# Performance work log

Measured on AMD Instinct MI355X. Metric: run time of the kernel, lower is better.

## Reference

```python
import jax, jax.numpy as jnp
import numpy as np

NUM_ENTITIES = 100000
NUM_RELATIONS = 500
D = 256            # embedding_dim
T = 4              # num_hash_tables
H = 32             # hash_dim
B = 64             # batch of queries
K = 10
CAND = max(K * 10, int(NUM_ENTITIES * 0.1))  # = 10000


def setup_inputs() -> dict:
    key = jax.random.key(0)
    k0, k1, k2, k3, k4 = jax.random.split(key, 5)
    return {
        "head": jax.random.randint(k0, (B,), 0, NUM_ENTITIES),
        "relation": jax.random.randint(k1, (B,), 0, NUM_RELATIONS),
        "entity_emb": jax.random.normal(k2, (NUM_ENTITIES, D), jnp.float32) * 0.02,
        "relation_emb": jax.random.normal(k3, (NUM_RELATIONS, D), jnp.float32) * 0.02,
        "hash_proj": jax.random.normal(k4, (T, D, H), jnp.float32),
        "k": K,
    }


def reference(head, relation, entity_emb, relation_emb, hash_proj, k):
    # DistMult approximate query path of KnowledgeGraph.query (use_approximate=True).
    h = entity_emb[head]            # [B, D]
    r = relation_emb[relation]      # [B, D]
    target = h * r                  # DistMult target embedding [B, D]

    # LSH hash codes (0/1 floats): projected > 0
    thash = (jnp.einsum('bd,tdh->bth', target, hash_proj) > 0).astype(jnp.float32)      # [B,T,H]
    ahash = (jnp.einsum('nd,tdh->nth', entity_emb, hash_proj) > 0).astype(jnp.float32)  # [N,T,H]

    # Hamming distance over (T,H) bits without materializing [B,N,T,H]:
    # mismatches = sum(a) + sum(b) - 2 * <a,b>  for 0/1 codes
    dot = jnp.einsum('bth,nth->bn', thash, ahash)                                        # [B,N]
    hash_dist = thash.sum((1, 2))[:, None] + ahash.sum((1, 2))[None, :] - 2.0 * dot      # [B,N]

    # top num_candidates with SMALLEST hamming distance
    _, cand_idx = jax.lax.top_k(-hash_dist, CAND)                                        # [B,CAND]

    # DistMult score: (h*r*t).sum(-1) == target . t ; compute dense then gather candidates
    scores_all = jnp.einsum('bd,nd->bn', target, entity_emb)                             # [B,N]
    cand_scores = jnp.take_along_axis(scores_all, cand_idx, axis=1)                      # [B,CAND]

    top_scores, top_local = jax.lax.top_k(cand_scores, k)                                # [B,k]
    top_indices = jnp.take_along_axis(cand_idx, top_local, axis=1)                       # [B,k]
    return top_indices, top_scores
```

## Files before the change

### kernel.cpp

```cpp
#include <hip/hip_runtime.h>
#include <hip/hip_bf16.h>
#include <float.h>

constexpr int NENT  = 100000;
constexpr int DDIM  = 256;
constexpr int BQ    = 64;
constexpr int CANDN = 10000;
constexpr int KTOP  = 10;
constexpr int NSLICE = 16;
constexpr int SLICE  = 6272;
constexpr int HPAD   = 132;

typedef short v8s __attribute__((ext_vector_type(8)));
typedef float v4f __attribute__((ext_vector_type(4)));

__device__ inline void split3(float x, unsigned short& h0, unsigned short& h1,
                              unsigned short& h2) {
    unsigned t0 = __float_as_uint(x) & 0xffff0000u;
    float r1 = x - __uint_as_float(t0);
    unsigned t1 = __float_as_uint(r1) & 0xffff0000u;
    float r2 = r1 - __uint_as_float(t1);
    h0 = (unsigned short)(t0 >> 16);
    h1 = (unsigned short)(t1 >> 16);
    h2 = (unsigned short)(__float_as_uint(r2) >> 16);
}

__device__ inline void split8(const float* ap, v8s& o0, v8s& o1, v8s& o2) {
    union { v8s v; unsigned short u[8]; } r0, r1, r2;
    float4 f0 = *(const float4*)ap;
    float4 f1 = *(const float4*)(ap + 4);
    float av[8] = {f0.x, f0.y, f0.z, f0.w, f1.x, f1.y, f1.z, f1.w};
    #pragma unroll
    for (int j = 0; j < 8; j++)
        split3(av[j], r0.u[j], r1.u[j], r2.u[j]);
    o0 = r0.v; o1 = r1.v; o2 = r2.v;
}

__global__ __launch_bounds__(128) void k_targets(
    const int* __restrict__ head, const int* __restrict__ rel,
    const float* __restrict__ E, const float* __restrict__ Rm,
    const float* __restrict__ proj,
    float* __restrict__ tgtT, unsigned* __restrict__ thash)
{
    __shared__ float tg[DDIM];
    int b = blockIdx.x;
    int tid = threadIdx.x;
    int h = head[b], r = rel[b];
    for (int d = tid; d < DDIM; d += 128) {
        float v = E[h*DDIM + d] * Rm[r*DDIM + d];
        tg[d] = v;
        tgtT[d*BQ + b] = v;
    }
    __syncthreads();
    int t = tid >> 5, hh = tid & 31;
    float acc = 0.f;
    #pragma unroll 8
    for (int d = 0; d < DDIM; d++)
        acc += tg[d] * proj[(t*DDIM + d)*32 + hh];
    unsigned long long m = __ballot(acc > 0.0f);
    int lane = tid & 63, w = tid >> 6;
    if (lane == 0) {
        thash[b*4 + w*2 + 0] = (unsigned)(m & 0xffffffffull);
        thash[b*4 + w*2 + 1] = (unsigned)(m >> 32);
    }
}

__global__ __launch_bounds__(256) void k_prepw(
    const float* __restrict__ proj, const float* __restrict__ tgtT,
    unsigned short* __restrict__ Whi, unsigned short* __restrict__ Wmid,
    unsigned short* __restrict__ Wlo)
{
    int c = blockIdx.x;
    int d = threadIdx.x;
    float x = (c < 128) ? proj[((c >> 5)*DDIM + d)*32 + (c & 31)]
                        : tgtT[d*BQ + (c - 128)];
    unsigned short h0, h1, h2;
    split3(x, h0, h1, h2);
    Whi [c*DDIM + d] = h0;
    Wmid[c*DDIM + d] = h1;
    Wlo [c*DDIM + d] = h2;
}

constexpr int TILE_E = 128;
constexpr int LSTR = 40;
constexpr int ASTR = 36;

__global__ __launch_bounds__(256, 2) void k_gemm(
    const float* __restrict__ E,
    const unsigned short* __restrict__ Whi, const unsigned short* __restrict__ Wmid,
    const unsigned short* __restrict__ Wlo,
    unsigned* __restrict__ ahash, float* __restrict__ scores)
{
    __shared__ __align__(16) float Af[TILE_E*ASTR];
    __shared__ __align__(16) unsigned short Bhi[192*LSTR];
    __shared__ __align__(16) unsigned short Bmid[192*LSTR];
    __shared__ __align__(16) unsigned short Blo[192*LSTR];
    unsigned short* bitsHalf = (unsigned short*)Af;

    int tid = threadIdx.x;
    int l = tid & 63, w = tid >> 6;
    int wm = w >> 1, wn = w & 1;
    int m = l & 15, quad = l >> 4;
    int n0 = blockIdx.x * TILE_E;

    v4f acc[4][6];
    #pragma unroll
    for (int a = 0; a < 4; a++)
        #pragma unroll
        for (int c = 0; c < 6; c++)
            acc[a][c] = (v4f)0.0f;

    for (int ch = 0; ch < DDIM/32; ch++) {
        int d0 = ch * 32;
        __syncthreads();
        #pragma unroll
        for (int it = 0; it < 4; it++) {
            int idx = tid + it*256;
            int row = idx >> 3;
            int kq  = (idx & 7) * 4;
            int n = n0 + row; if (n >= NENT) n = NENT - 1;
            *(float4*)&Af[row*ASTR + kq] = *(const float4*)(E + (size_t)n*DDIM + d0 + kq);
        }
        #pragma unroll
        for (int it = 0; it < 3; it++) {
            int idx = tid + it*256;
            int col = idx >> 2;
            int k8  = (idx & 3) * 8;
            *(uint4*)&Bhi [col*LSTR + k8] = *(const uint4*)(Whi  + col*DDIM + d0 + k8);
            *(uint4*)&Bmid[col*LSTR + k8] = *(const uint4*)(Wmid + col*DDIM + d0 + k8);
            *(uint4*)&Blo [col*LSTR + k8] = *(const uint4*)(Wlo  + col*DDIM + d0 + k8);
        }
        __syncthreads();
        v8s a0[4], a1[4], a2[4];
        #pragma unroll
        for (int a = 0; a < 4; a++)
            split8(&Af[(wm*64 + a*16 + m)*ASTR + quad*8], a0[a], a1[a], a2[a]);
        #pragma unroll
        for (int c = 0; c < 6; c++) {
            int co = (wn*96 + c*16 + m)*LSTR + quad*8;
            v8s b0 = *(const v8s*)&Bhi [co];
            v8s b1 = *(const v8s*)&Bmid[co];
            v8s b2 = *(const v8s*)&Blo [co];
            #pragma unroll
            for (int a = 0; a < 4; a++) {
                acc[a][c] = __builtin_amdgcn_mfma_f32_16x16x32_bf16(a2[a], b0, acc[a][c], 0, 0, 0);
                acc[a][c] = __builtin_amdgcn_mfma_f32_16x16x32_bf16(a0[a], b2, acc[a][c], 0, 0, 0);
                acc[a][c] = __builtin_amdgcn_mfma_f32_16x16x32_bf16(a1[a], b1, acc[a][c], 0, 0, 0);
                acc[a][c] = __builtin_amdgcn_mfma_f32_16x16x32_bf16(a1[a], b0, acc[a][c], 0, 0, 0);
                acc[a][c] = __builtin_amdgcn_mfma_f32_16x16x32_bf16(a0[a], b1, acc[a][c], 0, 0, 0);
                acc[a][c] = __builtin_amdgcn_mfma_f32_16x16x32_bf16(a0[a], b0, acc[a][c], 0, 0, 0);
            }
        }
    }

    __syncthreads();
    #pragma unroll
    for (int c = 0; c < 6; c++) {
        int ct = wn*6 + c;
        if (ct < 8) {
            #pragma unroll
            for (int a = 0; a < 4; a++) {
                #pragma unroll
                for (int r = 0; r < 4; r++) {
                    unsigned long long mb = __ballot(acc[a][c][r] > 0.0f);
                    if (m == 0) {
                        int rowl = wm*64 + a*16 + quad*4 + r;
                        bitsHalf[rowl*8 + ct] = (unsigned short)(mb >> (quad*16));
                    }
                }
            }
        } else {
            int b = ct*16 - 128 + m;
            #pragma unroll
            for (int a = 0; a < 4; a++) {
                int nb = n0 + wm*64 + a*16 + quad*4;
                if (nb < NENT)
                    *(float4*)(scores + (size_t)b*NENT + nb) = *(float4*)&acc[a][c];
            }
        }
    }
    __syncthreads();
    if (tid < TILE_E) {
        int n = n0 + tid;
        if (n < NENT)
            *(uint4*)(ahash + (size_t)n*4) = *(const uint4*)&bitsHalf[tid*8];
    }
}

__global__ __launch_bounds__(256) void k_dist(
    const unsigned* __restrict__ ahash, const unsigned* __restrict__ thash,
    unsigned char* __restrict__ dist8, unsigned short* __restrict__ histG)
{
    __shared__ unsigned hist[HPAD];
    int s = blockIdx.x, b = blockIdx.y, tid = threadIdx.x;
    for (int i = tid; i < HPAD; i += 256) hist[i] = 0u;
    uint4 tw = *(const uint4*)(thash + b*4);
    __syncthreads();
    int n0 = s*SLICE;
    int n1 = n0 + SLICE; if (n1 > NENT) n1 = NENT;
    unsigned char* drow = dist8 + (size_t)b*NENT;
    for (int n = n0 + tid*4; n < n1; n += 1024) {
        int dv[4];
        #pragma unroll
        for (int i = 0; i < 4; i++) {
            uint4 a = *(const uint4*)(ahash + (size_t)(n+i)*4);
            dv[i] = __popc(a.x^tw.x) + __popc(a.y^tw.y) +
                    __popc(a.z^tw.z) + __popc(a.w^tw.w);
            atomicAdd(&hist[dv[i]], 1u);
        }
        uchar4 o = make_uchar4((unsigned char)dv[0], (unsigned char)dv[1],
                               (unsigned char)dv[2], (unsigned char)dv[3]);
        *(uchar4*)(drow + n) = o;
    }
    __syncthreads();
    unsigned short* hrow = histG + ((size_t)b*NSLICE + s)*HPAD;
    for (int i = tid; i < 129; i += 256) hrow[i] = (unsigned short)hist[i];
}

__global__ __launch_bounds__(64) void k_cut(
    const unsigned char* __restrict__ dist8, const unsigned short* __restrict__ histG,
    int* __restrict__ dsG, int* __restrict__ ncG)
{
    __shared__ unsigned histT[HPAD];
    __shared__ int dsS, slS, rpS;
    int b = blockIdx.x, tid = threadIdx.x;
    for (int d = tid; d < 129; d += 64) {
        unsigned sum = 0;
        for (int s = 0; s < NSLICE; s++)
            sum += histG[((size_t)b*NSLICE + s)*HPAD + d];
        histT[d] = sum;
    }
    __syncthreads();
    if (tid == 0) {
        unsigned cum = 0; int ds = 128; unsigned R = 1;
        for (int d = 0; d < 129; d++) {
            unsigned c = cum + histT[d];
            if (c >= (unsigned)CANDN) { ds = d; R = (unsigned)CANDN - cum; break; }
            cum = c;
        }
        dsS = ds; dsG[b] = ds;
        unsigned acc = 0;
        for (int s = 0; s < NSLICE; s++) {
            unsigned c = histG[((size_t)b*NSLICE + s)*HPAD + ds];
            if (acc + c >= R) { slS = s; rpS = (int)(R - acc); break; }
            acc += c;
        }
    }
    __syncthreads();
    int ds = dsS;
    unsigned Rp = (unsigned)rpS;
    const unsigned char* drow = dist8 + (size_t)b*NENT;
    int sBase = slS*SLICE;
    int sEnd = sBase + SLICE; if (sEnd > NENT) sEnd = NENT;
    unsigned cnt = 0;
    for (int base = sBase; base < sEnd; base += 64) {
        int n = base + tid;
        bool eq = (n < sEnd) && (drow[n] == (unsigned char)ds);
        unsigned long long mm = __ballot(eq);
        unsigned c = __popcll(mm);
        if (cnt + c >= Rp) {
            unsigned pre = __popcll(mm & ((1ull << tid) - 1ull));
            if (eq && (cnt + pre + 1u == Rp)) ncG[b] = n;
            break;
        }
        cnt += c;
    }
}

__global__ __launch_bounds__(256) void k_part(
    const unsigned char* __restrict__ dist8, const float* __restrict__ scores,
    const int* __restrict__ dsG, const int* __restrict__ ncG,
    const float* __restrict__ tgtT, const float* __restrict__ E,
    float* __restrict__ partS, int* __restrict__ partI)
{
    __shared__ float rs[256];
    __shared__ int   ri[256];
    __shared__ int   rt[256];
    __shared__ int   chosenI[KTOP];
    __shared__ float tgl[DDIM];

    int sl = blockIdx.x, b = blockIdx.y, tid = threadIdx.x;
    int ds = dsG[b], nc = ncG[b];
    const unsigned char* drow = dist8 + (size_t)b*NENT;
    const float* srow = scores + (size_t)b*NENT;
    int n0 = sl*SLICE;
    int n1 = n0 + SLICE; if (n1 > NENT) n1 = NENT;

    float topS[KTOP]; int topI[KTOP];
    #pragma unroll
    for (int i = 0; i < KTOP; i++) { topS[i] = -FLT_MAX; topI[i] = 0x7fffffff; }

    for (int n = n0 + tid*4; n < n1; n += 1024) {
        uchar4 dv = *(const uchar4*)(drow + n);
        unsigned char da[4] = {dv.x, dv.y, dv.z, dv.w};
        #pragma unroll
        for (int i = 0; i < 4; i++) {
            int d = da[i];
            int nn = n + i;
            if (d < ds || (d == ds && nn <= nc)) {
                float sc = srow[nn];
                if (sc > topS[KTOP-1]) {
                    int p = KTOP - 1;
                    while (p > 0 && topS[p-1] < sc) {
                        topS[p] = topS[p-1]; topI[p] = topI[p-1]; p--;
                    }
                    topS[p] = sc; topI[p] = nn;
                }
            }
        }
    }

    int ph = 0;
    for (int r = 0; r < KTOP; r++) {
        rs[tid] = topS[ph]; ri[tid] = topI[ph]; rt[tid] = tid;
        __syncthreads();
        for (int st = 128; st > 0; st >>= 1) {
            if (tid < st) {
                bool take = (rs[tid+st] > rs[tid]) ||
                            (rs[tid+st] == rs[tid] && ri[tid+st] < ri[tid]);
                if (take) { rs[tid]=rs[tid+st]; ri[tid]=ri[tid+st]; rt[tid]=rt[tid+st]; }
            }
            __syncthreads();
        }
        if (tid == 0) {
            chosenI[r] = ri[0];
            partI[((size_t)b*NSLICE + sl)*KTOP + r] = ri[0];
        }
        int winner = rt[0];
        __syncthreads();
        if (tid == winner) ph++;
        __syncthreads();
    }

    for (int d = tid; d < DDIM; d += 256) tgl[d] = tgtT[d*BQ + b];
    __syncthreads();
    if (tid < KTOP) {
        int idx = chosenI[tid];
        float sc = -FLT_MAX;
        if (idx >= 0 && idx < NENT) {
            const float* er = E + (size_t)idx*DDIM;
            float acc = 0.f;
            #pragma unroll 8
            for (int d = 0; d < DDIM; d += 4) {
                float4 v = *(const float4*)(er + d);
                acc += v.x*tgl[d+0];
                acc += v.y*tgl[d+1];
                acc += v.z*tgl[d+2];
                acc += v.w*tgl[d+3];
            }
            sc = acc;
        }
        partS[((size_t)b*NSLICE + sl)*KTOP + tid] = sc;
    }
}

__global__ __launch_bounds__(256) void k_merge(
    const float* __restrict__ partS, const int* __restrict__ partI,
    float* __restrict__ out)
{
    __shared__ float sc2[NSLICE*KTOP];
    __shared__ int   ix2[NSLICE*KTOP];
    int b = blockIdx.x, tid = threadIdx.x;
    if (tid < NSLICE*KTOP) {
        sc2[tid] = partS[(size_t)b*NSLICE*KTOP + tid];
        ix2[tid] = partI[(size_t)b*NSLICE*KTOP + tid];
    }
    __syncthreads();
    if (tid < NSLICE*KTOP) {
        float mv = sc2[tid]; int mi = ix2[tid];
        int rank = 0;
        #pragma unroll 8
        for (int i = 0; i < NSLICE*KTOP; i++) {
            float v = sc2[i]; int id = ix2[i];
            bool beats = (v > mv) ||
                         (v == mv && (id < mi || (id == mi && i < tid)));
            rank += beats ? 1 : 0;
        }
        if (rank < KTOP) {
            out[b*KTOP + rank]           = (float)mi;
            out[BQ*KTOP + b*KTOP + rank] = mv;
        }
    }
}

extern "C" void kernel_launch(void* const* d_in, const int* in_sizes, int n_in,
                              void* d_out, int out_size, void* d_ws, size_t ws_size,
                              hipStream_t stream)
{
    const int*   head = (const int*)d_in[0];
    const int*   rel  = (const int*)d_in[1];
    const float* E    = (const float*)d_in[2];
    const float* Rm   = (const float*)d_in[3];
    const float* proj = (const float*)d_in[4];

    char* ws = (char*)d_ws;
    float*          tgtT   = (float*)(ws);
    unsigned*       thash  = (unsigned*)(ws + 65536);
    unsigned*       ahash  = (unsigned*)(ws + 66560);
    float*          scores = (float*)(ws + 1666560);
    unsigned char*  dist8  = (unsigned char*)(ws + 27266560);
    int*            dsG    = (int*)(ws + 33666560);
    int*            ncG    = (int*)(ws + 33666816);
    float*          partS  = (float*)(ws + 33667072);
    int*            partI  = (int*)(ws + 33708032);
    unsigned short* histG  = (unsigned short*)(ws + 33748992);
    unsigned short* Whi    = (unsigned short*)(ws + 34019328);
    unsigned short* Wmid   = (unsigned short*)(ws + 34117632);
    unsigned short* Wlo    = (unsigned short*)(ws + 34215936);
    float*          out    = (float*)d_out;

    hipLaunchKernelGGL(k_targets, dim3(BQ), dim3(128), 0, stream,
                       head, rel, E, Rm, proj, tgtT, thash);
    hipLaunchKernelGGL(k_prepw, dim3(192), dim3(256), 0, stream,
                       proj, tgtT, Whi, Wmid, Wlo);
    hipLaunchKernelGGL(k_gemm, dim3((NENT + TILE_E - 1)/TILE_E), dim3(256), 0, stream,
                       E, Whi, Wmid, Wlo, ahash, scores);
    hipLaunchKernelGGL(k_dist, dim3(NSLICE, BQ), dim3(256), 0, stream,
                       ahash, thash, dist8, histG);
    hipLaunchKernelGGL(k_cut, dim3(BQ), dim3(64), 0, stream,
                       dist8, histG, dsG, ncG);
    hipLaunchKernelGGL(k_part, dim3(NSLICE, BQ), dim3(256), 0, stream,
                       dist8, scores, dsG, ncG, tgtT, E, partS, partI);
    hipLaunchKernelGGL(k_merge, dim3(BQ), dim3(256), 0, stream,
                       partS, partI, out);
}
```

Before: 357.3 us.

## Load entity A-fragments directly from global into registers, skip LDS staging

The GEMM kernel no longer stages the entity tile in shared memory. Each lane loads its own A-fragment rows straight from global into registers before the barrier, and the B tiles are also prefetched into registers ahead of the sync. Shrinking LDS use lets the launch bound go from 2 to 3 blocks per SM, and the final barrier is dropped because bitsHalf now has its own buffer. The trade-offs are less coalesced A loads, since each lane reads 32 contiguous bytes per row, and higher register pressure that may spill at the tighter occupancy bound.

```diff
diff --git a/kernel.cpp b/kernel.cpp
--- a/kernel.cpp
+++ b/kernel.cpp
@@ -23,17 +23,6 @@
     h0 = (unsigned short)(t0 >> 16);
     h1 = (unsigned short)(t1 >> 16);
     h2 = (unsigned short)(__float_as_uint(r2) >> 16);
-}
-
-__device__ inline void split8(const float* ap, v8s& o0, v8s& o1, v8s& o2) {
-    union { v8s v; unsigned short u[8]; } r0, r1, r2;
-    float4 f0 = *(const float4*)ap;
-    float4 f1 = *(const float4*)(ap + 4);
-    float av[8] = {f0.x, f0.y, f0.z, f0.w, f1.x, f1.y, f1.z, f1.w};
-    #pragma unroll
-    for (int j = 0; j < 8; j++)
-        split3(av[j], r0.u[j], r1.u[j], r2.u[j]);
-    o0 = r0.v; o1 = r1.v; o2 = r2.v;
 }
 
 __global__ __launch_bounds__(128) void k_targets(
@@ -83,19 +72,17 @@
 
 constexpr int TILE_E = 128;
 constexpr int LSTR = 40;
-constexpr int ASTR = 36;
-
-__global__ __launch_bounds__(256, 2) void k_gemm(
+
+__global__ __launch_bounds__(256, 3) void k_gemm(
     const float* __restrict__ E,
     const unsigned short* __restrict__ Whi, const unsigned short* __restrict__ Wmid,
     const unsigned short* __restrict__ Wlo,
     unsigned* __restrict__ ahash, float* __restrict__ scores)
 {
-    __shared__ __align__(16) float Af[TILE_E*ASTR];
     __shared__ __align__(16) unsigned short Bhi[192*LSTR];
     __shared__ __align__(16) unsigned short Bmid[192*LSTR];
     __shared__ __align__(16) unsigned short Blo[192*LSTR];
-    unsigned short* bitsHalf = (unsigned short*)Af;
+    __shared__ __align__(16) unsigned short bitsHalf[TILE_E*8];
 
     int tid = threadIdx.x;
     int l = tid & 63, w = tid >> 6;
@@ -103,6 +90,16 @@
     int m = l & 15, quad = l >> 4;
     int n0 = blockIdx.x * TILE_E;
 
+    const float* arow[4];
+    #pragma unroll
+    for (int a = 0; a < 4; a++) {
+        int n = n0 + wm*64 + a*16 + m;
+        if (n >= NENT) n = NENT - 1;
+        arow[a] = E + (size_t)n*DDIM + quad*8;
+    }
+    int colS = tid >> 2;
+    int k8S  = (tid & 3) * 8;
+
     v4f acc[4][6];
     #pragma unroll
     for (int a = 0; a < 4; a++)
@@ -112,29 +109,40 @@
 
     for (int ch = 0; ch < DDIM/32; ch++) {
         int d0 = ch * 32;
+        float4 av[4][2];
+        #pragma unroll
+        for (int a = 0; a < 4; a++) {
+            av[a][0] = *(const float4*)(arow[a] + d0);
+            av[a][1] = *(const float4*)(arow[a] + d0 + 4);
+        }
+        uint4 bh[3], bm[3], bl[3];
+        #pragma unroll
+        for (int it = 0; it < 3; it++) {
+            int col = colS + it*64;
+            bh[it] = *(const uint4*)(Whi  + col*DDIM + d0 + k8S);
+            bm[it] = *(const uint4*)(Wmid + col*DDIM + d0 + k8S);
+            bl[it] = *(const uint4*)(Wlo  + col*DDIM + d0 + k8S);
+        }
         __syncthreads();
         #pragma unroll
-        for (int it = 0; it < 4; it++) {
-            int idx = tid + it*256;
-            int row = idx >> 3;
-            int kq  = (idx & 7) * 4;
-            int n = n0 + row; if (n >= NENT) n = NENT - 1;
-            *(float4*)&Af[row*ASTR + kq] = *(const float4*)(E + (size_t)n*DDIM + d0 + kq);
-        }
-        #pragma unroll
         for (int it = 0; it < 3; it++) {
-            int idx = tid + it*256;
-            int col = idx >> 2;
-            int k8  = (idx & 3) * 8;
-            *(uint4*)&Bhi [col*LSTR + k8] = *(const uint4*)(Whi  + col*DDIM + d0 + k8);
-            *(uint4*)&Bmid[col*LSTR + k8] = *(const uint4*)(Wmid + col*DDIM + d0 + k8);
-            *(uint4*)&Blo [col*LSTR + k8] = *(const uint4*)(Wlo  + col*DDIM + d0 + k8);
+            int col = colS + it*64;
+            *(uint4*)&Bhi [col*LSTR + k8S] = bh[it];
+            *(uint4*)&Bmid[col*LSTR + k8S] = bm[it];
+            *(uint4*)&Blo [col*LSTR + k8S] = bl[it];
         }
         __syncthreads();
         v8s a0[4], a1[4], a2[4];
         #pragma unroll
-        for (int a = 0; a < 4; a++)
-            split8(&Af[(wm*64 + a*16 + m)*ASTR + quad*8], a0[a], a1[a], a2[a]);
+        for (int a = 0; a < 4; a++) {
+            union { float4 f[2]; float s[8]; } u;
+            u.f[0] = av[a][0]; u.f[1] = av[a][1];
+            union { v8s v; unsigned short x[8]; } r0, r1, r2;
+            #pragma unroll
+            for (int j = 0; j < 8; j++)
+                split3(u.s[j], r0.x[j], r1.x[j], r2.x[j]);
+            a0[a] = r0.v; a1[a] = r1.v; a2[a] = r2.v;
+        }
         #pragma unroll
         for (int c = 0; c < 6; c++) {
             int co = (wn*96 + c*16 + m)*LSTR + quad*8;
@@ -153,7 +161,6 @@
         }
     }
 
-    __syncthreads();
     #pragma unroll
     for (int c = 0; c < 6; c++) {
         int ct = wn*6 + c;
```

After: 604.3 us. +69.1%, slower.
